# Kernel tuning notes

Measured on AMD Instinct MI355X. Metric: run time of the kernel, lower is better.

## Reference

```python
import jax, jax.numpy as jnp
import numpy as np

EPS = 1e-4


def setup_inputs() -> dict:
    key = jax.random.key(0)
    ks = jax.random.split(key, 16)
    N, D, H, K = 262144, 162, 256, 30
    s = 0.05  # weight init scale
    return {
        "Yh": jax.random.uniform(ks[0], (N, D), dtype=jnp.float32),
        "u": jax.random.uniform(ks[1], (1,), dtype=jnp.float32),
        "W1": jax.random.normal(ks[2], (D, H), dtype=jnp.float32) * s,
        "b1": jnp.zeros((H,), jnp.float32),
        "W2": jax.random.normal(ks[3], (H, H), dtype=jnp.float32) * s,
        "b2": jnp.zeros((H,), jnp.float32),
        "Wa": jax.random.normal(ks[4], (H, K), dtype=jnp.float32) * s,
        "ba": jnp.zeros((K,), jnp.float32),
        "Wb": jax.random.normal(ks[5], (H, K), dtype=jnp.float32) * s,
        "bb": jnp.zeros((K,), jnp.float32),
        "Wd1": jax.random.normal(ks[6], (K, H), dtype=jnp.float32) * s,
        "bd1": jnp.zeros((H,), jnp.float32),
        "Wd2": jax.random.normal(ks[7], (H, D), dtype=jnp.float32) * s,
        "bd2": jnp.zeros((D,), jnp.float32),
    }


def _stick_segments(v):
    # pi_k = v_k * prod_{j<k} (1 - v_j)  (vectorized exclusive cumprod,
    # replacing the original per-dim Python loop)
    cp = jnp.cumprod(1.0 - v, axis=1)  # [N, K]
    excl = jnp.concatenate([jnp.ones_like(v[:, :1]), cp[:, :-1]], axis=1)
    return v * excl


def reference(Yh, u, W1, b1, W2, b2, Wa, ba, Wb, bb, Wd1, bd1, Wd2, bd2):
    # encode_hsi: dense MLP -> positive Kumaraswamy params (softplus heads)
    h = jax.nn.relu(Yh @ W1 + b1)
    h = jax.nn.relu(h @ W2 + b2)
    alpha = jax.nn.softplus(h @ Wa + ba) + EPS  # param1_hsi [N, K]
    beta = jax.nn.softplus(h @ Wb + bb) + EPS   # param2_hsi [N, K]
    # Kumaraswamy reparametrization with a single shared uniform sample
    uu = u[0] * 0.98 + 0.01  # Uniform(0.01, 0.99) scalar
    v = (1.0 - uu ** (1.0 / beta)) ** (1.0 / alpha)  # [N, K]
    # set_v_K_to_one: force last stick proportion to 1
    v = jnp.concatenate([v[:, :-1], jnp.ones_like(v[:, :1])], axis=1)
    pi_h = _stick_segments(v)  # [N, K], rows sum to 1
    # decode: MLP -> sigmoid (positive outputs, recon.log() finite)
    d = jax.nn.relu(pi_h @ Wd1 + bd1)
    recon = jax.nn.sigmoid(d @ Wd2 + bd2)  # [N, D]
    return recon, alpha, beta, pi_h
```

## Files before the change

kernel.cpp:

```cpp
#include <hip/hip_runtime.h>
#include <hip/hip_bf16.h>

#define N_ROWS 262144
#define D_IN 162
#define K_DIM 30
#define ROWS 32

using bf16_t = __hip_bfloat16;
typedef __attribute__((ext_vector_type(8))) short bf16x8;
typedef __attribute__((ext_vector_type(4))) float f32x4;

__device__ __forceinline__ int swz_byte(int row, int col) {
  int b = (row << 9) + (col << 1);
  return b ^ ((row & 7) << 4);
}

__device__ __forceinline__ uint32_t bf16b(float x) {
  return (uint32_t)__builtin_bit_cast(unsigned short, __float2bfloat16(x));
}
__device__ __forceinline__ uint32_t pack2(float lo, float hi) {
  return bf16b(lo) | (bf16b(hi) << 16);
}

__device__ __forceinline__ float fexp2(float x) { return __builtin_amdgcn_exp2f(x); }
__device__ __forceinline__ float flog2(float x) { return __builtin_amdgcn_logf(x); }
__device__ __forceinline__ float frcp (float x) { return __builtin_amdgcn_rcpf(x); }

__device__ __forceinline__ float sp_fast(float x) {
  float e = fexp2(fabsf(x) * -1.44269504f);
  return fmaxf(x, 0.f) + 0.69314718f * flog2(1.f + e);
}
__device__ __forceinline__ float sigmoid_fast(float x) {
  return frcp(1.f + fexp2(x * -1.44269504f));
}

template<typename T> __device__ __forceinline__ void pin(T& x) {
  asm volatile("" : "+v"(x));
}

__global__ void pack_b_kernel(const float* __restrict__ src, bf16_t* __restrict__ dst,
                              int K, int N, int Np, int KB) {
  int idx = blockIdx.x * 256 + threadIdx.x;
  int total = KB * Np * 32;
  if (idx >= total) return;
  int ks = idx & 31;
  int n  = (idx >> 5) % Np;
  int kb = idx / (32 * Np);
  int k  = kb * 32 + ks;
  float v = (k < K && n < N) ? src[k * N + n] : 0.f;
  dst[idx] = __float2bfloat16(v);
}

__global__ void pack_ab_kernel(const float* __restrict__ Wa, const float* __restrict__ Wb,
                               bf16_t* __restrict__ dst) {
  int idx = blockIdx.x * 256 + threadIdx.x;
  if (idx >= 8 * 64 * 32) return;
  int ks = idx & 31;
  int n  = (idx >> 5) & 63;
  int kb = idx >> 11;
  int k  = kb * 32 + ks;
  int j = n >> 1, s = n & 1;
  float v = (j < K_DIM) ? (s ? Wb[k * K_DIM + j] : Wa[k * K_DIM + j]) : 0.f;
  dst[idx] = __float2bfloat16(v);
}

template<int NP, int NMO>
__device__ __forceinline__ void wload(const bf16_t* __restrict__ Wp, int kb, int ocBase,
                                      int lr, int lg, bf16x8 (&out)[NMO]) {
#pragma unroll
  for (int mo = 0; mo < NMO; ++mo)
    out[mo] = *reinterpret_cast<const bf16x8*>(
        Wp + ((kb * NP + ocBase + 16 * mo + lr) << 5) + 8 * lg);
}

template<int KB, int NP, int NMO>
__device__ __forceinline__ void gemm_roll(const uint8_t* lds, int srcOff,
                                          const bf16_t* __restrict__ Wp, int ocBase,
                                          int lr, int lg, f32x4 (&acc)[NMO][2],
                                          bf16x8 (&wbuf)[2][NMO]) {
  int bE[2], bO[2];
#pragma unroll
  for (int nr = 0; nr < 2; ++nr) {
    bE[nr] = srcOff + swz_byte(16 * nr + lr, 8 * lg);
    bO[nr] = srcOff + swz_byte(16 * nr + lr, 32 + 8 * lg);
  }
#pragma unroll
  for (int kb = 0; kb < KB; ++kb) {
    bf16x8 cur[NMO];
#pragma unroll
    for (int mo = 0; mo < NMO; ++mo) cur[mo] = wbuf[kb & 1][mo];
    if (kb + 2 < KB)
      wload<NP, NMO>(Wp, kb + 2, ocBase, lr, lg, wbuf[kb & 1]);
    bf16x8 hf[2];
#pragma unroll
    for (int nr = 0; nr < 2; ++nr) {
      int base = (kb & 1) ? bO[nr] : bE[nr];
      hf[nr] = *reinterpret_cast<const bf16x8*>(lds + base + (kb >> 1) * 128);
    }
#pragma unroll
    for (int mo = 0; mo < NMO; ++mo)
#pragma unroll
      for (int nr = 0; nr < 2; ++nr)
        acc[mo][nr] = __builtin_amdgcn_mfma_f32_16x16x32_bf16(cur[mo], hf[nr], acc[mo][nr], 0, 0, 0);
  }
}

template<int NMO>
__device__ __forceinline__ void acc_bias_init(const float* __restrict__ bias, int ocBase,
                                              int lg, f32x4 (&acc)[NMO][2]) {
#pragma unroll
  for (int mo = 0; mo < NMO; ++mo) {
    float4 bv = *reinterpret_cast<const float4*>(bias + ocBase + 16 * mo + 4 * lg);
    f32x4 t = {bv.x, bv.y, bv.z, bv.w};
#pragma unroll
    for (int nr = 0; nr < 2; ++nr) acc[mo][nr] = t;
  }
}

template<int NMO>
__device__ __forceinline__ void epi_relu_store(uint8_t* lds, int dstOff, int ocBase,
                                               int lr, int lg, f32x4 (&acc)[NMO][2]) {
#pragma unroll
  for (int mo = 0; mo < NMO; ++mo)
#pragma unroll
    for (int nr = 0; nr < 2; ++nr) {
      int row = 16 * nr + lr;
      int col = ocBase + 16 * mo + 4 * lg;
      float x0 = fmaxf(acc[mo][nr][0], 0.f), x1 = fmaxf(acc[mo][nr][1], 0.f);
      float x2 = fmaxf(acc[mo][nr][2], 0.f), x3 = fmaxf(acc[mo][nr][3], 0.f);
      uint2 p; p.x = pack2(x0, x1); p.y = pack2(x2, x3);
      *reinterpret_cast<uint2*>(lds + dstOff + swz_byte(row, col)) = p;
    }
}

template<int LG>
__device__ __forceinline__ bf16x8 scan_frag(const float* __restrict__ vrow,
                                            float* __restrict__ piOut) {
  float ex = 1.f, hold = 0.f;
  uint32_t pk0 = 0, pk1 = 0, pk2 = 0, pk3 = 0;
#pragma unroll
  for (int j = 0; j < 32; ++j) {
    float pi;
    if (j < K_DIM - 1)       { float vj = vrow[j]; pi = vj * ex; ex *= (1.f - vj); }
    else if (j == K_DIM - 1)   pi = ex;
    else                       pi = 0.f;
    if (piOut != nullptr && j < K_DIM) piOut[j] = pi;
    if (j >= 8 * LG && j < 8 * LG + 8) {
      if (j & 1) {
        uint32_t p = pack2(hold, pi);
        switch ((j - 8 * LG) >> 1) {
          case 0: pk0 = p; break; case 1: pk1 = p; break;
          case 2: pk2 = p; break; default: pk3 = p;
        }
      } else hold = pi;
    }
  }
  uint4 t = make_uint4(pk0, pk1, pk2, pk3);
  return __builtin_bit_cast(bf16x8, t);
}

#define OFF_B  16384
#define OFF_PI (16384 + 8192)

__launch_bounds__(256, 4)
__global__ void usdn_fused(const float* __restrict__ Yh, const float* __restrict__ u,
                           const float* __restrict__ b1, const float* __restrict__ b2,
                           const float* __restrict__ ba, const float* __restrict__ bb,
                           const float* __restrict__ bd1, const float* __restrict__ bd2,
                           const bf16_t* __restrict__ Wp1, const bf16_t* __restrict__ Wp2,
                           const bf16_t* __restrict__ Wpab, const bf16_t* __restrict__ Wpd1,
                           const bf16_t* __restrict__ Wpd2,
                           float* __restrict__ outRecon, float* __restrict__ outAlpha,
                           float* __restrict__ outBeta, float* __restrict__ outPi) {
  __shared__ __align__(16) uint8_t lds[32768];

  const int tid = threadIdx.x;
  const int w  = tid >> 6;
  const int l  = tid & 63;
  const int lr = l & 15;
  const int lg = l >> 4;
  const int r0 = blockIdx.x * ROWS;

  const int srow = tid >> 3, sl8 = tid & 7;
  float2 sv[12];
  {
    const float2* src = reinterpret_cast<const float2*>(Yh + (size_t)(r0 + srow) * D_IN);
#pragma unroll
    for (int it = 0; it < 12; ++it) {
      int f2 = sl8 + it * 8;
      if (f2 < 81) sv[it] = src[f2];
    }
  }
  bf16x8 w1buf[2][4];
  wload<256, 4>(Wp1, 0, w * 64, lr, lg, w1buf[0]);
  wload<256, 4>(Wp1, 1, w * 64, lr, lg, w1buf[1]);
#pragma unroll
  for (int mo = 0; mo < 4; ++mo) { pin(w1buf[0][mo]); pin(w1buf[1][mo]); }
  {
#pragma unroll
    for (int it = 0; it < 12; ++it) {
      int f2 = sl8 + it * 8;
      uint32_t p = 0;
      if (f2 < 81) p = pack2(sv[it].x, sv[it].y);
      if (f2 < 96) *reinterpret_cast<uint32_t*>(lds + swz_byte(srow, f2 * 2)) = p;
    }
  }
  __syncthreads();

  bf16x8 w2buf[2][4];
  {
    f32x4 acc[4][2];
    acc_bias_init<4>(b1, w * 64, lg, acc);
    gemm_roll<6, 256, 4>(lds, 0, Wp1, w * 64, lr, lg, acc, w1buf);
    wload<256, 4>(Wp2, 0, w * 64, lr, lg, w2buf[0]);
    wload<256, 4>(Wp2, 1, w * 64, lr, lg, w2buf[1]);
#pragma unroll
    for (int mo = 0; mo < 4; ++mo) { pin(w2buf[0][mo]); pin(w2buf[1][mo]); }
    epi_relu_store<4>(lds, OFF_B, w * 64, lr, lg, acc);
  }
  __syncthreads();

  bf16x8 wh[8];
  {
    f32x4 acc[4][2];
    acc_bias_init<4>(b2, w * 64, lg, acc);
    gemm_roll<8, 256, 4>(lds, OFF_B, Wp2, w * 64, lr, lg, acc, w2buf);
#pragma unroll
    for (int kb = 0; kb < 8; ++kb) {
      wh[kb] = *reinterpret_cast<const bf16x8*>(Wpab + ((kb * 64 + 16 * w + lr) << 5) + 8 * lg);
      pin(wh[kb]);
    }
    epi_relu_store<4>(lds, 0, w * 64, lr, lg, acc);
  }
  __syncthreads();

  float regA0[2], regA1[2], regB0[2], regB1[2];
  const int j0 = 8 * w + 2 * lg;
  bf16x8 w4[4];
  bf16x8 w5buf[2][3];
  {
    bool jv = (j0 < K_DIM);
    float ba0 = jv ? ba[j0] : 0.f,     bb0 = jv ? bb[j0] : 0.f;
    float ba1 = jv ? ba[j0 + 1] : 0.f, bb1 = jv ? bb[j0 + 1] : 0.f;
    f32x4 acc[2];
    f32x4 binit = {ba0, bb0, ba1, bb1};
    acc[0] = binit; acc[1] = binit;
    int bE[2], bO[2];
#pragma unroll
    for (int nr = 0; nr < 2; ++nr) {
      bE[nr] = swz_byte(16 * nr + lr, 8 * lg);
      bO[nr] = swz_byte(16 * nr + lr, 32 + 8 * lg);
    }
#pragma unroll
    for (int kb = 0; kb < 8; ++kb) {
#pragma unroll
      for (int nr = 0; nr < 2; ++nr) {
        int base = (kb & 1) ? bO[nr] : bE[nr];
        bf16x8 hf = *reinterpret_cast<const bf16x8*>(lds + base + (kb >> 1) * 128);
        acc[nr] = __builtin_amdgcn_mfma_f32_16x16x32_bf16(wh[kb], hf, acc[nr], 0, 0, 0);
      }
    }
    wload<256, 4>(Wpd1, 0, w * 64, lr, lg, w4);
    wload<192, 3>(Wpd2, 0, 48 * w, lr, lg, w5buf[0]);
    wload<192, 3>(Wpd2, 1, 48 * w, lr, lg, w5buf[1]);
#pragma unroll
    for (int mo = 0; mo < 4; ++mo) pin(w4[mo]);
#pragma unroll
    for (int mo = 0; mo < 3; ++mo) { pin(w5buf[0][mo]); pin(w5buf[1][mo]); }

    float uu  = u[0] * 0.98f + 0.01f;
    float l2u = flog2(uu);
    float* vbuf = reinterpret_cast<float*>(lds + OFF_B);
#pragma unroll
    for (int nr = 0; nr < 2; ++nr) {
      int row = 16 * nr + lr;
      float a0  = sp_fast(acc[nr][0]) + 1e-4f;
      float b0v = sp_fast(acc[nr][1]) + 1e-4f;
      float a1  = sp_fast(acc[nr][2]) + 1e-4f;
      float b1v = sp_fast(acc[nr][3]) + 1e-4f;
      regA0[nr] = a0; regB0[nr] = b0v; regA1[nr] = a1; regB1[nr] = b1v;
      if (jv) {
        if (j0 < K_DIM - 1) {
          float t = fexp2(l2u * frcp(b0v));
          vbuf[row * 36 + j0] = fexp2(flog2(1.f - t) * frcp(a0));
        }
        if (j0 + 1 < K_DIM - 1) {
          float t = fexp2(l2u * frcp(b1v));
          vbuf[row * 36 + j0 + 1] = fexp2(flog2(1.f - t) * frcp(a1));
        }
      }
    }
  }
  __syncthreads();

  {
    f32x4 acc[4][2];
    bf16x8 pf[2];
    const float* vb  = reinterpret_cast<const float*>(lds + OFF_B);
    float* piT = reinterpret_cast<float*>(lds + OFF_PI);
#pragma unroll
    for (int nr = 0; nr < 2; ++nr) {
      int row = 16 * nr + lr;
      const float* vrow = vb + row * 36;
      float* po = (w == 0) ? (piT + row * 34) : nullptr;
      if      (lg == 0) pf[nr] = scan_frag<0>(vrow, po);
      else if (lg == 1) pf[nr] = scan_frag<1>(vrow, nullptr);
      else if (lg == 2) pf[nr] = scan_frag<2>(vrow, nullptr);
      else              pf[nr] = scan_frag<3>(vrow, nullptr);
    }
    acc_bias_init<4>(bd1, w * 64, lg, acc);
#pragma unroll
    for (int mo = 0; mo < 4; ++mo)
#pragma unroll
      for (int nr = 0; nr < 2; ++nr)
        acc[mo][nr] = __builtin_amdgcn_mfma_f32_16x16x32_bf16(w4[mo], pf[nr], acc[mo][nr], 0, 0, 0);
    epi_relu_store<4>(lds, 0, w * 64, lr, lg, acc);
  }
  __syncthreads();

  {
    f32x4 acc[3][2];
#pragma unroll
    for (int mo = 0; mo < 3; ++mo) {
      int col0 = 48 * w + 16 * mo + 4 * lg;
      f32x4 t;
#pragma unroll
      for (int i = 0; i < 4; ++i) t[i] = (col0 + i < D_IN) ? bd2[col0 + i] : 0.f;
#pragma unroll
      for (int nr = 0; nr < 2; ++nr) acc[mo][nr] = t;
    }
    gemm_roll<8, 192, 3>(lds, 0, Wpd2, 48 * w, lr, lg, acc, w5buf);
#pragma unroll
    for (int mo = 0; mo < 3; ++mo) {
      int col0 = 48 * w + 16 * mo + 4 * lg;
#pragma unroll
      for (int nr = 0; nr < 2; ++nr) {
        int row = 16 * nr + lr;
        float s0 = sigmoid_fast(acc[mo][nr][0]);
        float s1 = sigmoid_fast(acc[mo][nr][1]);
        float s2 = sigmoid_fast(acc[mo][nr][2]);
        float s3 = sigmoid_fast(acc[mo][nr][3]);
        float* dst = outRecon + (size_t)(r0 + row) * D_IN + col0;
        if (col0 < D_IN)     *reinterpret_cast<float2*>(dst)     = make_float2(s0, s1);
        if (col0 + 2 < D_IN) *reinterpret_cast<float2*>(dst + 2) = make_float2(s2, s3);
      }
    }
  }

  if (j0 < K_DIM) {
#pragma unroll
    for (int nr = 0; nr < 2; ++nr) {
      int row = 16 * nr + lr;
      size_t base = (size_t)(r0 + row) * K_DIM + j0;
      *reinterpret_cast<float2*>(outAlpha + base) = make_float2(regA0[nr], regA1[nr]);
      *reinterpret_cast<float2*>(outBeta  + base) = make_float2(regB0[nr], regB1[nr]);
    }
  }
  {
    const float* piT = reinterpret_cast<const float*>(lds + OFF_PI);
    int row = tid >> 3, l8 = tid & 7;
#pragma unroll
    for (int half = 0; half < 2; ++half) {
      int f2 = l8 + half * 8;
      if (f2 < 15) {
        float2 pp = *reinterpret_cast<const float2*>(piT + row * 34 + f2 * 2);
        *reinterpret_cast<float2*>(outPi + (size_t)(r0 + row) * K_DIM + f2 * 2) = pp;
      }
    }
  }
}

extern "C" void kernel_launch(void* const* d_in, const int* in_sizes, int n_in,
                              void* d_out, int out_size, void* d_ws, size_t ws_size,
                              hipStream_t stream) {
  const float* Yh  = (const float*)d_in[0];
  const float* u   = (const float*)d_in[1];
  const float* W1  = (const float*)d_in[2];
  const float* b1  = (const float*)d_in[3];
  const float* W2  = (const float*)d_in[4];
  const float* b2  = (const float*)d_in[5];
  const float* Wa  = (const float*)d_in[6];
  const float* ba  = (const float*)d_in[7];
  const float* Wb  = (const float*)d_in[8];
  const float* bb  = (const float*)d_in[9];
  const float* Wd1 = (const float*)d_in[10];
  const float* bd1 = (const float*)d_in[11];
  const float* Wd2 = (const float*)d_in[12];
  const float* bd2 = (const float*)d_in[13];

  bf16_t* ws   = (bf16_t*)d_ws;
  bf16_t* Wp1  = ws;
  bf16_t* Wp2  = Wp1 + 49152;
  bf16_t* Wpab = Wp2 + 65536;
  bf16_t* Wpd1 = Wpab + 16384;
  bf16_t* Wpd2 = Wpd1 + 8192;

  float* outRecon = (float*)d_out;
  float* outAlpha = outRecon + (size_t)N_ROWS * D_IN;
  float* outBeta  = outAlpha + (size_t)N_ROWS * K_DIM;
  float* outPi    = outBeta  + (size_t)N_ROWS * K_DIM;

  pack_b_kernel<<<192, 256, 0, stream>>>(W1, Wp1, 162, 256, 256, 6);
  pack_b_kernel<<<256, 256, 0, stream>>>(W2, Wp2, 256, 256, 256, 8);
  pack_ab_kernel<<<64, 256, 0, stream>>>(Wa, Wb, Wpab);
  pack_b_kernel<<<32, 256, 0, stream>>>(Wd1, Wpd1, 30, 256, 256, 1);
  pack_b_kernel<<<192, 256, 0, stream>>>(Wd2, Wpd2, 256, 162, 192, 8);

  usdn_fused<<<N_ROWS / ROWS, 256, 0, stream>>>(Yh, u, b1, b2, ba, bb, bd1, bd2,
                                                Wp1, Wp2, Wpab, Wpd1, Wpd2,
                                                outRecon, outAlpha, outBeta, outPi);
}
```

Before: 277.6 us.

## Drop weight register prefetch and shrink LDS to double occupancy

Removes the register-resident double-buffered weight prefetching and the pinned weight fragments, loading weights directly each k-step. LDS is reduced to about 19 KB by reusing one buffer for activations, v values and the scan, with extra barriers. Pi is stashed in LDS as bf16 pairs. Launch bounds rise to 8 blocks per CU so more waves can hide latency. The trade-off is exposed global weight-load latency in each GEMM step, more barriers, and a bf16-rounded pi_h output.

```diff
diff --git a/kernel.cpp b/kernel.cpp
--- a/kernel.cpp
+++ b/kernel.cpp
@@ -21,6 +21,12 @@
 __device__ __forceinline__ uint32_t pack2(float lo, float hi) {
   return bf16b(lo) | (bf16b(hi) << 16);
 }
+__device__ __forceinline__ float unpk_lo(uint32_t p) {
+  return __bfloat162float(__builtin_bit_cast(__hip_bfloat16, (unsigned short)(p & 0xffff)));
+}
+__device__ __forceinline__ float unpk_hi(uint32_t p) {
+  return __bfloat162float(__builtin_bit_cast(__hip_bfloat16, (unsigned short)(p >> 16)));
+}
 
 __device__ __forceinline__ float fexp2(float x) { return __builtin_amdgcn_exp2f(x); }
 __device__ __forceinline__ float flog2(float x) { return __builtin_amdgcn_logf(x); }
@@ -32,10 +38,6 @@
 }
 __device__ __forceinline__ float sigmoid_fast(float x) {
   return frcp(1.f + fexp2(x * -1.44269504f));
-}
-
-template<typename T> __device__ __forceinline__ void pin(T& x) {
-  asm volatile("" : "+v"(x));
 }
 
 __global__ void pack_b_kernel(const float* __restrict__ src, bf16_t* __restrict__ dst,
@@ -74,10 +76,9 @@
 }
 
 template<int KB, int NP, int NMO>
-__device__ __forceinline__ void gemm_roll(const uint8_t* lds, int srcOff,
-                                          const bf16_t* __restrict__ Wp, int ocBase,
-                                          int lr, int lg, f32x4 (&acc)[NMO][2],
-                                          bf16x8 (&wbuf)[2][NMO]) {
+__device__ __forceinline__ void gemm_direct(const uint8_t* lds, int srcOff,
+                                            const bf16_t* __restrict__ Wp, int ocBase,
+                                            int lr, int lg, f32x4 (&acc)[NMO][2]) {
   int bE[2], bO[2];
 #pragma unroll
   for (int nr = 0; nr < 2; ++nr) {
@@ -86,11 +87,8 @@
   }
 #pragma unroll
   for (int kb = 0; kb < KB; ++kb) {
-    bf16x8 cur[NMO];
-#pragma unroll
-    for (int mo = 0; mo < NMO; ++mo) cur[mo] = wbuf[kb & 1][mo];
-    if (kb + 2 < KB)
-      wload<NP, NMO>(Wp, kb + 2, ocBase, lr, lg, wbuf[kb & 1]);
+    bf16x8 wf[NMO];
+    wload<NP, NMO>(Wp, kb, ocBase, lr, lg, wf);
     bf16x8 hf[2];
 #pragma unroll
     for (int nr = 0; nr < 2; ++nr) {
@@ -101,7 +99,7 @@
     for (int mo = 0; mo < NMO; ++mo)
 #pragma unroll
       for (int nr = 0; nr < 2; ++nr)
-        acc[mo][nr] = __builtin_amdgcn_mfma_f32_16x16x32_bf16(cur[mo], hf[nr], acc[mo][nr], 0, 0, 0);
+        acc[mo][nr] = __builtin_amdgcn_mfma_f32_16x16x32_bf16(wf[mo], hf[nr], acc[mo][nr], 0, 0, 0);
   }
 }
 
@@ -135,7 +133,7 @@
 
 template<int LG>
 __device__ __forceinline__ bf16x8 scan_frag(const float* __restrict__ vrow,
-                                            float* __restrict__ piOut) {
+                                            uint8_t* __restrict__ piPair) {
   float ex = 1.f, hold = 0.f;
   uint32_t pk0 = 0, pk1 = 0, pk2 = 0, pk3 = 0;
 #pragma unroll
@@ -144,25 +142,25 @@
     if (j < K_DIM - 1)       { float vj = vrow[j]; pi = vj * ex; ex *= (1.f - vj); }
     else if (j == K_DIM - 1)   pi = ex;
     else                       pi = 0.f;
-    if (piOut != nullptr && j < K_DIM) piOut[j] = pi;
-    if (j >= 8 * LG && j < 8 * LG + 8) {
-      if (j & 1) {
-        uint32_t p = pack2(hold, pi);
+    if (j & 1) {
+      uint32_t p = pack2(hold, pi);
+      if (piPair != nullptr && j < K_DIM)
+        *reinterpret_cast<uint32_t*>(piPair + (j - 1) * 2) = p;
+      if (j >= 8 * LG && j < 8 * LG + 8) {
         switch ((j - 8 * LG) >> 1) {
           case 0: pk0 = p; break; case 1: pk1 = p; break;
           case 2: pk2 = p; break; default: pk3 = p;
         }
-      } else hold = pi;
-    }
+      }
+    } else hold = pi;
   }
   uint4 t = make_uint4(pk0, pk1, pk2, pk3);
   return __builtin_bit_cast(bf16x8, t);
 }
 
-#define OFF_B  16384
-#define OFF_PI (16384 + 8192)
-
-__launch_bounds__(256, 4)
+#define OFF_PI 16384
+
+__launch_bounds__(256, 8)
 __global__ void usdn_fused(const float* __restrict__ Yh, const float* __restrict__ u,
                            const float* __restrict__ b1, const float* __restrict__ b2,
                            const float* __restrict__ ba, const float* __restrict__ bb,
@@ -172,7 +170,7 @@
                            const bf16_t* __restrict__ Wpd2,
                            float* __restrict__ outRecon, float* __restrict__ outAlpha,
                            float* __restrict__ outBeta, float* __restrict__ outPi) {
-  __shared__ __align__(16) uint8_t lds[32768];
+  __shared__ __align__(16) uint8_t lds[18944];
 
   const int tid = threadIdx.x;
   const int w  = tid >> 6;
@@ -181,139 +179,108 @@
   const int lg = l >> 4;
   const int r0 = blockIdx.x * ROWS;
 
-  const int srow = tid >> 3, sl8 = tid & 7;
-  float2 sv[12];
-  {
+  {
+    const int srow = tid >> 3, sl8 = tid & 7;
     const float2* src = reinterpret_cast<const float2*>(Yh + (size_t)(r0 + srow) * D_IN);
 #pragma unroll
-    for (int it = 0; it < 12; ++it) {
-      int f2 = sl8 + it * 8;
-      if (f2 < 81) sv[it] = src[f2];
-    }
-  }
-  bf16x8 w1buf[2][4];
-  wload<256, 4>(Wp1, 0, w * 64, lr, lg, w1buf[0]);
-  wload<256, 4>(Wp1, 1, w * 64, lr, lg, w1buf[1]);
-#pragma unroll
-  for (int mo = 0; mo < 4; ++mo) { pin(w1buf[0][mo]); pin(w1buf[1][mo]); }
-  {
-#pragma unroll
-    for (int it = 0; it < 12; ++it) {
-      int f2 = sl8 + it * 8;
-      uint32_t p = 0;
-      if (f2 < 81) p = pack2(sv[it].x, sv[it].y);
-      if (f2 < 96) *reinterpret_cast<uint32_t*>(lds + swz_byte(srow, f2 * 2)) = p;
-    }
-  }
-  __syncthreads();
-
-  bf16x8 w2buf[2][4];
+    for (int h = 0; h < 2; ++h) {
+      float2 sv[6];
+#pragma unroll
+      for (int it = 0; it < 6; ++it) {
+        int f2 = sl8 + (h * 6 + it) * 8;
+        if (f2 < 81) sv[it] = src[f2];
+      }
+#pragma unroll
+      for (int it = 0; it < 6; ++it) {
+        int f2 = sl8 + (h * 6 + it) * 8;
+        uint32_t p = 0;
+        if (f2 < 81) p = pack2(sv[it].x, sv[it].y);
+        if (f2 < 96) *reinterpret_cast<uint32_t*>(lds + swz_byte(srow, f2 * 2)) = p;
+      }
+    }
+  }
+  __syncthreads();
+
   {
     f32x4 acc[4][2];
     acc_bias_init<4>(b1, w * 64, lg, acc);
-    gemm_roll<6, 256, 4>(lds, 0, Wp1, w * 64, lr, lg, acc, w1buf);
-    wload<256, 4>(Wp2, 0, w * 64, lr, lg, w2buf[0]);
-    wload<256, 4>(Wp2, 1, w * 64, lr, lg, w2buf[1]);
-#pragma unroll
-    for (int mo = 0; mo < 4; ++mo) { pin(w2buf[0][mo]); pin(w2buf[1][mo]); }
-    epi_relu_store<4>(lds, OFF_B, w * 64, lr, lg, acc);
-  }
-  __syncthreads();
-
-  bf16x8 wh[8];
+    gemm_direct<6, 256, 4>(lds, 0, Wp1, w * 64, lr, lg, acc);
+    __syncthreads();
+    epi_relu_store<4>(lds, 0, w * 64, lr, lg, acc);
+  }
+  __syncthreads();
+
   {
     f32x4 acc[4][2];
     acc_bias_init<4>(b2, w * 64, lg, acc);
-    gemm_roll<8, 256, 4>(lds, OFF_B, Wp2, w * 64, lr, lg, acc, w2buf);
-#pragma unroll
-    for (int kb = 0; kb < 8; ++kb) {
-      wh[kb] = *reinterpret_cast<const bf16x8*>(Wpab + ((kb * 64 + 16 * w + lr) << 5) + 8 * lg);
-      pin(wh[kb]);
-    }
+    gemm_direct<8, 256, 4>(lds, 0, Wp2, w * 64, lr, lg, acc);
+    __syncthreads();
     epi_relu_store<4>(lds, 0, w * 64, lr, lg, acc);
   }
   __syncthreads();
 
   float regA0[2], regA1[2], regB0[2], regB1[2];
   const int j0 = 8 * w + 2 * lg;
-  bf16x8 w4[4];
-  bf16x8 w5buf[2][3];
   {
     bool jv = (j0 < K_DIM);
     float ba0 = jv ? ba[j0] : 0.f,     bb0 = jv ? bb[j0] : 0.f;
     float ba1 = jv ? ba[j0 + 1] : 0.f, bb1 = jv ? bb[j0 + 1] : 0.f;
-    f32x4 acc[2];
+    f32x4 acc[1][2];
     f32x4 binit = {ba0, bb0, ba1, bb1};
-    acc[0] = binit; acc[1] = binit;
-    int bE[2], bO[2];
-#pragma unroll
-    for (int nr = 0; nr < 2; ++nr) {
-      bE[nr] = swz_byte(16 * nr + lr, 8 * lg);
-      bO[nr] = swz_byte(16 * nr + lr, 32 + 8 * lg);
-    }
-#pragma unroll
-    for (int kb = 0; kb < 8; ++kb) {
-#pragma unroll
-      for (int nr = 0; nr < 2; ++nr) {
-        int base = (kb & 1) ? bO[nr] : bE[nr];
-        bf16x8 hf = *reinterpret_cast<const bf16x8*>(lds + base + (kb >> 1) * 128);
-        acc[nr] = __builtin_amdgcn_mfma_f32_16x16x32_bf16(wh[kb], hf, acc[nr], 0, 0, 0);
-      }
-    }
-    wload<256, 4>(Wpd1, 0, w * 64, lr, lg, w4);
-    wload<192, 3>(Wpd2, 0, 48 * w, lr, lg, w5buf[0]);
-    wload<192, 3>(Wpd2, 1, 48 * w, lr, lg, w5buf[1]);
-#pragma unroll
-    for (int mo = 0; mo < 4; ++mo) pin(w4[mo]);
-#pragma unroll
-    for (int mo = 0; mo < 3; ++mo) { pin(w5buf[0][mo]); pin(w5buf[1][mo]); }
+    acc[0][0] = binit; acc[0][1] = binit;
+    gemm_direct<8, 64, 1>(lds, 0, Wpab, 16 * w, lr, lg, acc);
 
     float uu  = u[0] * 0.98f + 0.01f;
     float l2u = flog2(uu);
-    float* vbuf = reinterpret_cast<float*>(lds + OFF_B);
+    float vv[2][2];
+#pragma unroll
+    for (int nr = 0; nr < 2; ++nr) {
+      float a0  = sp_fast(acc[0][nr][0]) + 1e-4f;
+      float b0v = sp_fast(acc[0][nr][1]) + 1e-4f;
+      float a1  = sp_fast(acc[0][nr][2]) + 1e-4f;
+      float b1v = sp_fast(acc[0][nr][3]) + 1e-4f;
+      regA0[nr] = a0; regB0[nr] = b0v; regA1[nr] = a1; regB1[nr] = b1v;
+      float t0 = fexp2(l2u * frcp(b0v));
+      vv[nr][0] = fexp2(flog2(1.f - t0) * frcp(a0));
+      float t1 = fexp2(l2u * frcp(b1v));
+      vv[nr][1] = fexp2(flog2(1.f - t1) * frcp(a1));
+    }
+    __syncthreads();
+    float* vbuf = reinterpret_cast<float*>(lds);
+    if (jv) {
+#pragma unroll
+      for (int nr = 0; nr < 2; ++nr) {
+        int row = 16 * nr + lr;
+        if (j0 < K_DIM - 1)     vbuf[row * 33 + j0]     = vv[nr][0];
+        if (j0 + 1 < K_DIM - 1) vbuf[row * 33 + j0 + 1] = vv[nr][1];
+      }
+    }
+  }
+  __syncthreads();
+
+  {
+    bf16x8 pf[2];
+    const float* vb = reinterpret_cast<const float*>(lds);
 #pragma unroll
     for (int nr = 0; nr < 2; ++nr) {
       int row = 16 * nr + lr;
-      float a0  = sp_fast(acc[nr][0]) + 1e-4f;
-      float b0v = sp_fast(acc[nr][1]) + 1e-4f;
-      float a1  = sp_fast(acc[nr][2]) + 1e-4f;
-      float b1v = sp_fast(acc[nr][3]) + 1e-4f;
-      regA0[nr] = a0; regB0[nr] = b0v; regA1[nr] = a1; regB1[nr] = b1v;
-      if (jv) {
-        if (j0 < K_DIM - 1) {
-          float t = fexp2(l2u * frcp(b0v));
-          vbuf[row * 36 + j0] = fexp2(flog2(1.f - t) * frcp(a0));
-        }
-        if (j0 + 1 < K_DIM - 1) {
-          float t = fexp2(l2u * frcp(b1v));
-          vbuf[row * 36 + j0 + 1] = fexp2(flog2(1.f - t) * frcp(a1));
-        }
-      }
-    }
-  }
-  __syncthreads();
-
-  {
-    f32x4 acc[4][2];
-    bf16x8 pf[2];
-    const float* vb  = reinterpret_cast<const float*>(lds + OFF_B);
-    float* piT = reinterpret_cast<float*>(lds + OFF_PI);
-#pragma unroll
-    for (int nr = 0; nr < 2; ++nr) {
-      int row = 16 * nr + lr;
-      const float* vrow = vb + row * 36;
-      float* po = (w == 0) ? (piT + row * 34) : nullptr;
+      const float* vrow = vb + row * 33;
+      uint8_t* po = (w == 0) ? (lds + OFF_PI + row * 80) : nullptr;
       if      (lg == 0) pf[nr] = scan_frag<0>(vrow, po);
       else if (lg == 1) pf[nr] = scan_frag<1>(vrow, nullptr);
       else if (lg == 2) pf[nr] = scan_frag<2>(vrow, nullptr);
       else              pf[nr] = scan_frag<3>(vrow, nullptr);
     }
+    f32x4 acc[4][2];
     acc_bias_init<4>(bd1, w * 64, lg, acc);
+    bf16x8 w4[4];
+    wload<256, 4>(Wpd1, 0, w * 64, lr, lg, w4);
 #pragma unroll
     for (int mo = 0; mo < 4; ++mo)
 #pragma unroll
       for (int nr = 0; nr < 2; ++nr)
         acc[mo][nr] = __builtin_amdgcn_mfma_f32_16x16x32_bf16(w4[mo], pf[nr], acc[mo][nr], 0, 0, 0);
+    __syncthreads();
     epi_relu_store<4>(lds, 0, w * 64, lr, lg, acc);
   }
   __syncthreads();
@@ -329,7 +296,7 @@
 #pragma unroll
       for (int nr = 0; nr < 2; ++nr) acc[mo][nr] = t;
     }
-    gemm_roll<8, 192, 3>(lds, 0, Wpd2, 48 * w, lr, lg, acc, w5buf);
+    gemm_direct<8, 192, 3>(lds, 0, Wpd2, 48 * w, lr, lg, acc);
 #pragma unroll
     for (int mo = 0; mo < 3; ++mo) {
       int col0 = 48 * w + 16 * mo + 4 * lg;
@@ -357,14 +324,14 @@
     }
   }
   {
-    const float* piT = reinterpret_cast<const float*>(lds + OFF_PI);
     int row = tid >> 3, l8 = tid & 7;
 #pragma unroll
     for (int half = 0; half < 2; ++half) {
       int f2 = l8 + half * 8;
       if (f2 < 15) {
-        float2 pp = *reinterpret_cast<const float2*>(piT + row * 34 + f2 * 2);
-        *reinterpret_cast<float2*>(outPi + (size_t)(r0 + row) * K_DIM + f2 * 2) = pp;
+        uint32_t pp = *reinterpret_cast<const uint32_t*>(lds + OFF_PI + row * 80 + f2 * 4);
+        *reinterpret_cast<float2*>(outPi + (size_t)(r0 + row) * K_DIM + f2 * 2) =
+            make_float2(unpk_lo(pp), unpk_hi(pp));
       }
     }
   }
```

Result: slower. 379.3 us (+36.6%).
